# Kernel tuning notes

Hardware: AMD Instinct MI355X
Metric: run time of the kernel (lower is better)

## Reference

```python
import jax, jax.numpy as jnp
import numpy as np

B, T, D, H = 4, 1024, 1024, 16
NUM_BUCKETS = 320
MAX_DIST = 800
LN_EPS = 1e-5


def _rel_bucket(T):
    # bidirectional T5-style relative position buckets
    ctx = jnp.arange(T)[:, None]
    mem = jnp.arange(T)[None, :]
    rel = mem - ctx  # (T, T)
    half = NUM_BUCKETS // 2  # 160
    bucket = (rel > 0).astype(jnp.int32) * half
    n = jnp.abs(rel)
    max_exact = half // 2  # 80
    is_small = n < max_exact
    n_f = jnp.maximum(n, 1).astype(jnp.float32)
    large = max_exact + (
        jnp.log(n_f / max_exact) / np.log(MAX_DIST / max_exact) * (half - max_exact)
    ).astype(jnp.int32)
    large = jnp.minimum(large, half - 1)
    return bucket + jnp.where(is_small, n, large)


def setup_inputs() -> dict:
    key = jax.random.key(0)
    ks = jax.random.split(key, 12)
    s = 0.02
    return {
        "x": jax.random.normal(ks[0], (B, T, D), jnp.float32),
        "ln_w": jnp.ones((D,), jnp.float32),
        "ln_b": jnp.zeros((D,), jnp.float32),
        "wq": jax.random.normal(ks[1], (D, D), jnp.float32) * s,
        "bq": jnp.zeros((D,), jnp.float32),
        "wk": jax.random.normal(ks[2], (D, D), jnp.float32) * s,
        "bk": jnp.zeros((D,), jnp.float32),
        "wv": jax.random.normal(ks[3], (D, D), jnp.float32) * s,
        "bv": jnp.zeros((D,), jnp.float32),
        "wo": jax.random.normal(ks[4], (D, D), jnp.float32) * s,
        "bo": jnp.zeros((D,), jnp.float32),
        "rel_emb": jax.random.normal(ks[5], (NUM_BUCKETS, H), jnp.float32) * s,
        "grep_w": jax.random.normal(ks[6], (8, D // H), jnp.float32) * s,
        "grep_b": jnp.zeros((8,), jnp.float32),
        "grep_a": jnp.ones((1, H, 1, 1), jnp.float32),
    }


def reference(x, ln_w, ln_b, wq, bq, wk, bk, wv, bv, wo, bo, rel_emb, grep_w, grep_b, grep_a):
    Bb, Tt, Dd = x.shape
    hd = Dd // H
    scaling = hd ** -0.5
    # pre-norm LayerNorm
    mu = jnp.mean(x, -1, keepdims=True)
    var = jnp.mean((x - mu) ** 2, -1, keepdims=True)
    h = (x - mu) / jnp.sqrt(var + LN_EPS) * ln_w + ln_b
    # projections (q pre-scaled as in fairseq/WavLM)
    q = (h @ wq.T + bq) * scaling
    k = h @ wk.T + bk
    v = h @ wv.T + bv
    q = q.reshape(Bb, Tt, H, hd).transpose(0, 2, 1, 3)  # (B,H,T,hd)
    k = k.reshape(Bb, Tt, H, hd).transpose(0, 2, 1, 3)
    v = v.reshape(Bb, Tt, H, hd).transpose(0, 2, 1, 3)
    # bucketed relative position bias: (H, T, T)
    buckets = _rel_bucket(Tt)
    pos_bias = rel_emb[buckets].transpose(2, 0, 1)
    # gru_rel_pos gating (per batch, head, query position)
    alpha = 32.0
    ql = q * (alpha / scaling)  # undo scaling, multiply by alpha
    g = jax.nn.sigmoid((ql @ grep_w.T + grep_b).reshape(Bb, H, Tt, 2, 4).sum(-1))
    gate_a, gate_b = g[..., 0:1], g[..., 1:2]  # (B,H,T,1)
    gate = gate_a * (gate_b * grep_a - 1.0) + 2.0
    # attention
    scores = jnp.einsum('bhtd,bhsd->bhts', q, k) + gate * pos_bias[None]
    attn = jax.nn.softmax(scores, axis=-1)
    out = jnp.einsum('bhts,bhsd->bhtd', attn, v).transpose(0, 2, 1, 3).reshape(Bb, Tt, Dd)
    # output projection, dropout (identity in eval), residual
    out = out @ wo.T + bo + x
    pos_bias_out = jnp.broadcast_to(pos_bias[None], (Bb, H, Tt, Tt)).reshape(Bb * H, Tt, Tt)
    return out, pos_bias_out
```

## Files before the change

### kernel.cpp

```cpp
#include <hip/hip_runtime.h>

typedef unsigned short u16;
typedef __attribute__((ext_vector_type(8))) short short8;
typedef __attribute__((ext_vector_type(4))) float floatx4;

#define MFMA16(a, b, c) __builtin_amdgcn_mfma_f32_16x16x32_bf16(a, b, c, 0, 0, 0)

#define GLL16(gp, lp)                                                              \
  __builtin_amdgcn_global_load_lds(                                                \
      (const __attribute__((address_space(1))) void*)(gp),                         \
      (__attribute__((address_space(3))) void*)(lp), 16, 0, 0)

__device__ __forceinline__ float bf2f(u16 u) {
  return __uint_as_float(((unsigned int)u) << 16);
}
__device__ __forceinline__ u16 f2bf(float f) {
  unsigned int u = __float_as_uint(f);
  unsigned int r = (u + 0x7fffu + ((u >> 16) & 1u)) >> 16;
  return (u16)r;
}

__global__ __launch_bounds__(256) void ln_kernel(
    const float* __restrict__ x, const float* __restrict__ w, const float* __restrict__ bb,
    u16* __restrict__ hb)
{
  int wid = threadIdx.x >> 6, lane = threadIdx.x & 63;
  int row = blockIdx.x * 4 + wid;
  const float* xr = x + row * 1024 + lane * 16;
  float xs[16];
#pragma unroll
  for (int i = 0; i < 4; i++) {
    float4 v = *(const float4*)(xr + i * 4);
    xs[i * 4 + 0] = v.x; xs[i * 4 + 1] = v.y; xs[i * 4 + 2] = v.z; xs[i * 4 + 3] = v.w;
  }
  float s = 0.f, ss = 0.f;
#pragma unroll
  for (int i = 0; i < 16; i++) { s += xs[i]; ss += xs[i] * xs[i]; }
#pragma unroll
  for (int m = 1; m < 64; m <<= 1) { s += __shfl_xor(s, m, 64); ss += __shfl_xor(ss, m, 64); }
  float mu = s * (1.0f / 1024.0f);
  float var = ss * (1.0f / 1024.0f) - mu * mu;
  float rstd = rsqrtf(var + 1e-5f);
  const float* wr = w + lane * 16;
  const float* br = bb + lane * 16;
  short8 o0, o1;
#pragma unroll
  for (int i = 0; i < 8; i++) {
    o0[i] = (short)f2bf((xs[i] - mu) * rstd * wr[i] + br[i]);
    o1[i] = (short)f2bf((xs[8 + i] - mu) * rstd * wr[8 + i] + br[8 + i]);
  }
  u16* hr = hb + row * 1024 + lane * 16;
  *(short8*)hr = o0;
  *(short8*)(hr + 8) = o1;
}

__device__ __forceinline__ int rel_bucket(int t, int s) {
  int rel = s - t;
  int bucket = (rel > 0) ? 160 : 0;
  int n = (rel < 0) ? -rel : rel;
  if (n < 80) return bucket + n;
  float a = logf((float)n / 80.0f);
  float c = a / (float)2.302585092994046;
  float v = c * 80.0f;
  int large = 80 + (int)v;
  if (large > 159) large = 159;
  return bucket + large;
}

__global__ __launch_bounds__(256) void convw_kernel(
    const float* __restrict__ wq, const float* __restrict__ wk,
    const float* __restrict__ wv, const float* __restrict__ wo,
    u16* __restrict__ wb, const float* __restrict__ rel_emb, float* __restrict__ tbl)
{
  int bid = blockIdx.x;
  if (bid >= 2048) {
    int idx = (bid - 2048) * 256 + threadIdx.x;
    int h = idx & 15, ri = idx >> 4;
    float v = 0.f;
    if (ri < 2047) {
      int rel = ri - 1023;
      v = rel_emb[rel_bucket(0, rel) * 16 + h];
    }
    tbl[h * 2048 + ri] = v;
    return;
  }
  int idx = (bid * 256 + threadIdx.x) * 8;
  int seg = idx >> 20, off = idx & 1048575;
  const float* s = (seg == 0) ? wq : (seg == 1) ? wk : (seg == 2) ? wv : wo;
  float4 f0 = *(const float4*)(s + off);
  float4 f1 = *(const float4*)(s + off + 4);
  short8 o;
  o[0] = (short)f2bf(f0.x); o[1] = (short)f2bf(f0.y);
  o[2] = (short)f2bf(f0.z); o[3] = (short)f2bf(f0.w);
  o[4] = (short)f2bf(f1.x); o[5] = (short)f2bf(f1.y);
  o[6] = (short)f2bf(f1.z); o[7] = (short)f2bf(f1.w);
  *(short8*)&wb[idx] = o;
}

__global__ __launch_bounds__(256) void qkv_kernel(
    const u16* __restrict__ hb, const u16* __restrict__ wb,
    const float* __restrict__ bq, const float* __restrict__ bk, const float* __restrict__ bv,
    u16* __restrict__ qs, u16* __restrict__ kko, u16* __restrict__ vn)
{
  __shared__ __align__(16) u16 As[128 * 32];
  __shared__ __align__(16) u16 Bs[128 * 32];
  int tid = threadIdx.x;
  int wid = tid >> 6, lane = tid & 63;
  int wm = wid >> 1, wn = wid & 1;
  int l15 = lane & 15, quad = lane >> 4;
  int m0 = blockIdx.y * 128;
  int n0g = blockIdx.x * 128;
  int sec = n0g >> 10;
  int n0 = n0g & 1023;
  const u16* W = wb + sec * 1048576;
  const float* bias = (sec == 0) ? bq : ((sec == 1) ? bk : bv);

  floatx4 zero4 = {0.f, 0.f, 0.f, 0.f};
  floatx4 acc[4][4];
#pragma unroll
  for (int i = 0; i < 4; i++)
#pragma unroll
    for (int j = 0; j < 4; j++) acc[i][j] = zero4;

  int lr = tid >> 2;
  int lc = (tid & 3) * 8;
  const u16* ga0 = &hb[(m0 + lr) * 1024 + lc];
  const u16* ga1 = &hb[(m0 + lr + 64) * 1024 + lc];
  const u16* gb0 = &W[(n0 + lr) * 1024 + lc];
  const u16* gb1 = &W[(n0 + lr + 64) * 1024 + lc];
  u16* la0 = &As[lr * 32 + lc];
  u16* la1 = &As[(lr + 64) * 32 + lc];
  u16* lb0 = &Bs[lr * 32 + lc];
  u16* lb1 = &Bs[(lr + 64) * 32 + lc];

  for (int kt = 0; kt < 1024; kt += 32) {
    GLL16(ga0 + kt, la0);
    GLL16(ga1 + kt, la1);
    GLL16(gb0 + kt, lb0);
    GLL16(gb1 + kt, lb1);
    __syncthreads();
    short8 af[4], bf[4];
#pragma unroll
    for (int mi = 0; mi < 4; mi++)
      af[mi] = *(const short8*)&As[(wm * 64 + mi * 16 + l15) * 32 + quad * 8];
#pragma unroll
    for (int ni = 0; ni < 4; ni++)
      bf[ni] = *(const short8*)&Bs[(wn * 64 + ni * 16 + l15) * 32 + quad * 8];
#pragma unroll
    for (int mi = 0; mi < 4; mi++)
#pragma unroll
      for (int ni = 0; ni < 4; ni++)
        acc[mi][ni] = MFMA16(af[mi], bf[ni], acc[mi][ni]);
    __syncthreads();
  }

  int bidx = m0 >> 10;
#pragma unroll
  for (int mi = 0; mi < 4; mi++) {
#pragma unroll
    for (int ni = 0; ni < 4; ni++) {
#pragma unroll
      for (int r = 0; r < 4; r++) {
        int row = m0 + wm * 64 + mi * 16 + quad * 4 + r;
        int t = row & 1023;
        int c = n0 + wn * 64 + ni * 16 + l15;
        float val = acc[mi][ni][r] + bias[c];
        int hh = c >> 6, hp = c & 63;
        if (sec == 0) {
          val *= 0.125f;
          qs[((bidx * 16 + hh) * 1024 + t) * 64 + hp] = f2bf(val);
        } else if (sec == 1) {
          kko[((bidx * 16 + hh) * 1024 + t) * 64 + hp] = f2bf(val);
        } else {
          vn[((bidx * 16 + hh) * 1024 + t) * 64 + hp] = f2bf(val);
        }
      }
    }
  }
}

__global__ __launch_bounds__(256) void vtrans_kernel(
    const u16* __restrict__ vn, u16* __restrict__ vt)
{
  __shared__ u16 Ts[64 * 72];
  int bh = blockIdx.x >> 4;
  int t0 = (blockIdx.x & 15) * 64;
  int tid = threadIdx.x;
  int row = tid >> 2;
  int c16 = (tid & 3) * 16;
  const u16* src = vn + bh * 65536 + (t0 + row) * 64 + c16;
  *(short8*)&Ts[row * 72 + c16]     = *(const short8*)&src[0];
  *(short8*)&Ts[row * 72 + c16 + 8] = *(const short8*)&src[8];
  __syncthreads();
  short8 o0, o1;
#pragma unroll
  for (int j = 0; j < 8; j++) {
    o0[j] = (short)Ts[(c16 + j) * 72 + row];
    o1[j] = (short)Ts[(c16 + 8 + j) * 72 + row];
  }
  u16* dst = vt + bh * 65536 + row * 1024 + t0 + c16;
  *(short8*)&dst[0] = o0;
  *(short8*)&dst[8] = o1;
}

__global__ __launch_bounds__(256) void attn_kernel(
    const u16* __restrict__ qs, const u16* __restrict__ kko, const u16* __restrict__ vt,
    const float* __restrict__ gw, const float* __restrict__ gb, const float* __restrict__ ga,
    const float* __restrict__ tbl, u16* __restrict__ ao)
{
  __shared__ __align__(16) u16 Pb[4][2 * 768];
  int wid = threadIdx.x >> 6, lane = threadIdx.x & 63;
  int l15 = lane & 15, quad = lane >> 4;
  int bh = blockIdx.x;
  int b = bh >> 4, h = bh & 15;
  int q0 = blockIdx.y * 64 + wid * 16;
  const u16* Q = qs + bh * 65536;
  const u16* K = kko + bh * 65536;
  const u16* V = vt + bh * 65536;
  u16* pbase = &Pb[wid][0];

  const u16* qrow = Q + (q0 + l15) * 64;
  float e[8];
#pragma unroll
  for (int i = 0; i < 8; i++) e[i] = 0.f;
  {
    short8 qa = *(const short8*)&qrow[quad * 16];
    short8 qc = *(const short8*)&qrow[quad * 16 + 8];
#pragma unroll
    for (int jj = 0; jj < 8; jj++) {
      float qla = bf2f((u16)qa[jj]) * 256.0f;
      float qlb = bf2f((u16)qc[jj]) * 256.0f;
      int j = quad * 16 + jj;
#pragma unroll
      for (int i = 0; i < 8; i++) {
        e[i] += qla * gw[i * 64 + j];
        e[i] += qlb * gw[i * 64 + j + 8];
      }
    }
  }
#pragma unroll
  for (int i = 0; i < 8; i++) {
    e[i] += __shfl_xor(e[i], 16, 64);
    e[i] += __shfl_xor(e[i], 32, 64);
  }
  float u0 = e[0] + e[1] + e[2] + e[3] + gb[0] + gb[1] + gb[2] + gb[3];
  float u1 = e[4] + e[5] + e[6] + e[7] + gb[4] + gb[5] + gb[6] + gb[7];
  float sa = 1.0f / (1.0f + __expf(-u0));
  float sc_ = 1.0f / (1.0f + __expf(-u1));
  float gv = sa * (sc_ * ga[h] - 1.0f) + 2.0f;

  short8 qf0 = *(const short8*)&Q[(q0 + l15) * 64 + quad * 8];
  short8 qf1 = *(const short8*)&Q[(q0 + l15) * 64 + quad * 8 + 32];

  const float* tb = tbl + h * 2048 + 1023 + quad * 4 - (q0 + l15);

  float mrun = -1e30f, lrun = 0.f;
  floatx4 zero4 = {0.f, 0.f, 0.f, 0.f};
  floatx4 accO[4];
#pragma unroll
  for (int ni = 0; ni < 4; ni++) accO[ni] = zero4;

  const u16* Kr = K + l15 * 64 + quad * 8;
  short8 ka0 = *(const short8*)&Kr[0];
  short8 ka1 = *(const short8*)&Kr[32];
  short8 kb0 = *(const short8*)&Kr[16 * 64];
  short8 kb1 = *(const short8*)&Kr[16 * 64 + 32];
  float bt[8];
#pragma unroll
  for (int r = 0; r < 4; r++) { bt[r] = tb[r]; bt[4 + r] = tb[16 + r]; }

  for (int it = 0; it < 32; it++) {
    int s0 = it * 32;
    floatx4 sc0 = zero4, sc1 = zero4;
    sc0 = MFMA16(ka0, qf0, sc0);
    sc0 = MFMA16(ka1, qf1, sc0);
    sc1 = MFMA16(kb0, qf0, sc1);
    sc1 = MFMA16(kb1, qf1, sc1);

    int sn = (s0 + 32) & 1023;
    const u16* Kn = K + (sn + l15) * 64 + quad * 8;
    short8 na0 = *(const short8*)&Kn[0];
    short8 na1 = *(const short8*)&Kn[32];
    short8 nb0 = *(const short8*)&Kn[16 * 64];
    short8 nb1 = *(const short8*)&Kn[16 * 64 + 32];
    float btn[8];
#pragma unroll
    for (int r = 0; r < 4; r++) { btn[r] = tb[sn + r]; btn[4 + r] = tb[sn + 16 + r]; }
    short8 vf0 = *(const short8*)&V[(0 * 16 + l15) * 1024 + s0 + quad * 8];
    short8 vf1 = *(const short8*)&V[(1 * 16 + l15) * 1024 + s0 + quad * 8];
    short8 vf2 = *(const short8*)&V[(2 * 16 + l15) * 1024 + s0 + quad * 8];
    short8 vf3 = *(const short8*)&V[(3 * 16 + l15) * 1024 + s0 + quad * 8];

    float vv[8];
#pragma unroll
    for (int r = 0; r < 4; r++) {
      vv[r]     = sc0[r] + gv * bt[r];
      vv[4 + r] = sc1[r] + gv * bt[4 + r];
    }
    float mt = fmaxf(fmaxf(fmaxf(vv[0], vv[1]), fmaxf(vv[2], vv[3])),
                     fmaxf(fmaxf(vv[4], vv[5]), fmaxf(vv[6], vv[7])));
    mt = fmaxf(mt, __shfl_xor(mt, 16, 64));
    mt = fmaxf(mt, __shfl_xor(mt, 32, 64));
    float mnew = fmaxf(mrun, mt);
    float al = __expf(fmaxf(mrun - mnew, -80.0f));
    float p[8], ps = 0.f;
#pragma unroll
    for (int j = 0; j < 8; j++) { p[j] = __expf(vv[j] - mnew); ps += p[j]; }
    ps += __shfl_xor(ps, 16, 64);
    ps += __shfl_xor(ps, 32, 64);
    lrun = lrun * al + ps;
    mrun = mnew;

    float ar[4];
#pragma unroll
    for (int r = 0; r < 4; r++) ar[r] = __shfl(al, quad * 4 + r, 64);
#pragma unroll
    for (int ni = 0; ni < 4; ni++) {
      floatx4 t = accO[ni];
      t[0] *= ar[0]; t[1] *= ar[1]; t[2] *= ar[2]; t[3] *= ar[3];
      accO[ni] = t;
    }

    unsigned w0, w1, w2, w3;
    asm("v_cvt_pk_bf16_f32 %0, %1, %2" : "=v"(w0) : "v"(p[0]), "v"(p[1]));
    asm("v_cvt_pk_bf16_f32 %0, %1, %2" : "=v"(w1) : "v"(p[2]), "v"(p[3]));
    asm("v_cvt_pk_bf16_f32 %0, %1, %2" : "=v"(w2) : "v"(p[4]), "v"(p[5]));
    asm("v_cvt_pk_bf16_f32 %0, %1, %2" : "=v"(w3) : "v"(p[6]), "v"(p[7]));
    u16* pw = pbase + (it & 1) * 768;
    uint2 wa; wa.x = w0; wa.y = w1;
    uint2 wbv; wbv.x = w2; wbv.y = w3;
    *(uint2*)&pw[l15 * 48 + quad * 4] = wa;
    *(uint2*)&pw[l15 * 48 + 16 + quad * 4] = wbv;
    asm volatile("s_waitcnt lgkmcnt(0)" ::: "memory");
    __builtin_amdgcn_sched_barrier(0);
    short8 pf = *(const short8*)&pw[l15 * 48 + quad * 8];

    accO[0] = MFMA16(pf, vf0, accO[0]);
    accO[1] = MFMA16(pf, vf1, accO[1]);
    accO[2] = MFMA16(pf, vf2, accO[2]);
    accO[3] = MFMA16(pf, vf3, accO[3]);

    ka0 = na0; ka1 = na1; kb0 = nb0; kb1 = nb1;
#pragma unroll
    for (int j = 0; j < 8; j++) bt[j] = btn[j];
  }

#pragma unroll
  for (int r = 0; r < 4; r++) {
    float lr = __shfl(lrun, quad * 4 + r, 64);
    float rl = 1.0f / lr;
    int t = q0 + quad * 4 + r;
#pragma unroll
    for (int ni = 0; ni < 4; ni++) {
      ao[(b * 1024 + t) * 1024 + h * 64 + ni * 16 + l15] = f2bf(accO[ni][r] * rl);
    }
  }
}

__global__ __launch_bounds__(256) void oproj_kernel(
    const u16* __restrict__ ao, const u16* __restrict__ wob, const float* __restrict__ bo,
    const float* __restrict__ x, float* __restrict__ out)
{
  __shared__ __align__(16) u16 As[128 * 32];
  __shared__ __align__(16) u16 Bs[128 * 32];
  int tid = threadIdx.x;
  int wid = tid >> 6, lane = tid & 63;
  int wm = wid >> 1, wn = wid & 1;
  int l15 = lane & 15, quad = lane >> 4;
  int m0 = blockIdx.y * 128;
  int n0 = blockIdx.x * 128;

  floatx4 zero4 = {0.f, 0.f, 0.f, 0.f};
  floatx4 acc[4][4];
#pragma unroll
  for (int i = 0; i < 4; i++)
#pragma unroll
    for (int j = 0; j < 4; j++) acc[i][j] = zero4;

  int lr = tid >> 2;
  int lc = (tid & 3) * 8;
  const u16* ga0 = &ao[(m0 + lr) * 1024 + lc];
  const u16* ga1 = &ao[(m0 + lr + 64) * 1024 + lc];
  const u16* gb0 = &wob[(n0 + lr) * 1024 + lc];
  const u16* gb1 = &wob[(n0 + lr + 64) * 1024 + lc];
  u16* la0 = &As[lr * 32 + lc];
  u16* la1 = &As[(lr + 64) * 32 + lc];
  u16* lb0 = &Bs[lr * 32 + lc];
  u16* lb1 = &Bs[(lr + 64) * 32 + lc];

  for (int kt = 0; kt < 1024; kt += 32) {
    GLL16(ga0 + kt, la0);
    GLL16(ga1 + kt, la1);
    GLL16(gb0 + kt, lb0);
    GLL16(gb1 + kt, lb1);
    __syncthreads();
    short8 af[4], bf[4];
#pragma unroll
    for (int mi = 0; mi < 4; mi++)
      af[mi] = *(const short8*)&As[(wm * 64 + mi * 16 + l15) * 32 + quad * 8];
#pragma unroll
    for (int ni = 0; ni < 4; ni++)
      bf[ni] = *(const short8*)&Bs[(wn * 64 + ni * 16 + l15) * 32 + quad * 8];
#pragma unroll
    for (int mi = 0; mi < 4; mi++)
#pragma unroll
      for (int ni = 0; ni < 4; ni++)
        acc[mi][ni] = MFMA16(af[mi], bf[ni], acc[mi][ni]);
    __syncthreads();
  }

#pragma unroll
  for (int mi = 0; mi < 4; mi++) {
#pragma unroll
    for (int ni = 0; ni < 4; ni++) {
#pragma unroll
      for (int r = 0; r < 4; r++) {
        int row = m0 + wm * 64 + mi * 16 + quad * 4 + r;
        int c = n0 + wn * 64 + ni * 16 + l15;
        out[row * 1024 + c] = acc[mi][ni][r] + bo[c] + x[row * 1024 + c];
      }
    }
  }
}

__global__ __launch_bounds__(256) void bias_all_kernel(
    const float* __restrict__ rel_emb, float* __restrict__ out1)
{
  int tid = blockIdx.x * 256 + threadIdx.x;
  int t = tid >> 7;
  int s0 = (tid & 127) * 8;
  int bkt[8];
#pragma unroll
  for (int j = 0; j < 8; j++) bkt[j] = rel_bucket(t, s0 + j) * 16;
  int base_ts = t * 1024 + s0;
#pragma unroll
  for (int hh = 0; hh < 16; hh++) {
    float4 v0, v1;
    v0.x = rel_emb[bkt[0] + hh]; v0.y = rel_emb[bkt[1] + hh];
    v0.z = rel_emb[bkt[2] + hh]; v0.w = rel_emb[bkt[3] + hh];
    v1.x = rel_emb[bkt[4] + hh]; v1.y = rel_emb[bkt[5] + hh];
    v1.z = rel_emb[bkt[6] + hh]; v1.w = rel_emb[bkt[7] + hh];
    float* p = out1 + hh * 1048576 + base_ts;
    *(float4*)p = v0;              *(float4*)(p + 4) = v1;
    *(float4*)(p + 16777216) = v0; *(float4*)(p + 16777216 + 4) = v1;
    *(float4*)(p + 33554432) = v0; *(float4*)(p + 33554432 + 4) = v1;
    *(float4*)(p + 50331648) = v0; *(float4*)(p + 50331648 + 4) = v1;
  }
}

extern "C" void kernel_launch(void* const* d_in, const int* in_sizes, int n_in,
                              void* d_out, int out_size, void* d_ws, size_t ws_size,
                              hipStream_t stream) {
  const float* x    = (const float*)d_in[0];
  const float* ln_w = (const float*)d_in[1];
  const float* ln_b = (const float*)d_in[2];
  const float* wq   = (const float*)d_in[3];
  const float* bq   = (const float*)d_in[4];
  const float* wk   = (const float*)d_in[5];
  const float* bk   = (const float*)d_in[6];
  const float* wv   = (const float*)d_in[7];
  const float* bv   = (const float*)d_in[8];
  const float* wo   = (const float*)d_in[9];
  const float* bo   = (const float*)d_in[10];
  const float* rel  = (const float*)d_in[11];
  const float* gw   = (const float*)d_in[12];
  const float* gb   = (const float*)d_in[13];
  const float* ga   = (const float*)d_in[14];

  float* out0  = (float*)d_out;
  float* out1f = out0 + 4194304;

  u16* hbb  = (u16*)(out1f + 16777216);
  u16* wbb  = (u16*)(out1f + 18874368);
  u16* qsb  = (u16*)(out1f + 20971520);
  u16* kkb  = (u16*)(out1f + 23068672);
  u16* vnb  = (u16*)(out1f + 25165824);
  u16* vtb  = (u16*)(out1f + 27262976);
  u16* aob  = (u16*)(out1f + 29360128);
  float* tbl =        out1f + 31457280;

  ln_kernel<<<1024, 256, 0, stream>>>(x, ln_w, ln_b, hbb);
  convw_kernel<<<2176, 256, 0, stream>>>(wq, wk, wv, wo, wbb, rel, tbl);
  qkv_kernel<<<dim3(24, 32), 256, 0, stream>>>(hbb, wbb, bq, bk, bv, qsb, kkb, vnb);
  vtrans_kernel<<<1024, 256, 0, stream>>>(vnb, vtb);
  attn_kernel<<<dim3(64, 16), 256, 0, stream>>>(qsb, kkb, vtb, gw, gb, ga, tbl, aob);
  oproj_kernel<<<dim3(8, 32), 256, 0, stream>>>(aob, wbb + 3145728, bo, x, out0);
  bias_all_kernel<<<512, 256, 0, stream>>>(rel, out1f);
}
```

Baseline: 524.6 us.

## Merge LayerNorm into prep kernel, skip softmax rescale, use workspace scratch

Folds the LayerNorm kernel into the weight-conversion/table kernel as extra blocks, removing one launch. Adds a lazy-rescale path in attention: when the new tile max exceeds the running max by at most 8 across the wave, the accumulator rescale and max update are skipped. Intermediate buffers move to the provided workspace when it is large enough, instead of living past the end of the output buffer. The lazy rescale lets unnormalised exponentials grow by up to e^8, which trades a little precision headroom for fewer multiplies and shuffles.

```diff
diff --git a/kernel.cpp b/kernel.cpp
--- a/kernel.cpp
+++ b/kernel.cpp
@@ -18,40 +18,6 @@
   unsigned int u = __float_as_uint(f);
   unsigned int r = (u + 0x7fffu + ((u >> 16) & 1u)) >> 16;
   return (u16)r;
-}
-
-__global__ __launch_bounds__(256) void ln_kernel(
-    const float* __restrict__ x, const float* __restrict__ w, const float* __restrict__ bb,
-    u16* __restrict__ hb)
-{
-  int wid = threadIdx.x >> 6, lane = threadIdx.x & 63;
-  int row = blockIdx.x * 4 + wid;
-  const float* xr = x + row * 1024 + lane * 16;
-  float xs[16];
-#pragma unroll
-  for (int i = 0; i < 4; i++) {
-    float4 v = *(const float4*)(xr + i * 4);
-    xs[i * 4 + 0] = v.x; xs[i * 4 + 1] = v.y; xs[i * 4 + 2] = v.z; xs[i * 4 + 3] = v.w;
-  }
-  float s = 0.f, ss = 0.f;
-#pragma unroll
-  for (int i = 0; i < 16; i++) { s += xs[i]; ss += xs[i] * xs[i]; }
-#pragma unroll
-  for (int m = 1; m < 64; m <<= 1) { s += __shfl_xor(s, m, 64); ss += __shfl_xor(ss, m, 64); }
-  float mu = s * (1.0f / 1024.0f);
-  float var = ss * (1.0f / 1024.0f) - mu * mu;
-  float rstd = rsqrtf(var + 1e-5f);
-  const float* wr = w + lane * 16;
-  const float* br = bb + lane * 16;
-  short8 o0, o1;
-#pragma unroll
-  for (int i = 0; i < 8; i++) {
-    o0[i] = (short)f2bf((xs[i] - mu) * rstd * wr[i] + br[i]);
-    o1[i] = (short)f2bf((xs[8 + i] - mu) * rstd * wr[8 + i] + br[8 + i]);
-  }
-  u16* hr = hb + row * 1024 + lane * 16;
-  *(short8*)hr = o0;
-  *(short8*)(hr + 8) = o1;
 }
 
 __device__ __forceinline__ int rel_bucket(int t, int s) {
@@ -67,12 +33,45 @@
   return bucket + large;
 }
 
-__global__ __launch_bounds__(256) void convw_kernel(
+__global__ __launch_bounds__(256) void prep_kernel(
     const float* __restrict__ wq, const float* __restrict__ wk,
     const float* __restrict__ wv, const float* __restrict__ wo,
-    u16* __restrict__ wb, const float* __restrict__ rel_emb, float* __restrict__ tbl)
+    u16* __restrict__ wb, const float* __restrict__ rel_emb, float* __restrict__ tbl,
+    const float* __restrict__ x, const float* __restrict__ ln_w, const float* __restrict__ ln_b,
+    u16* __restrict__ hb)
 {
   int bid = blockIdx.x;
+  if (bid >= 2176) {
+    int wid = threadIdx.x >> 6, lane = threadIdx.x & 63;
+    int row = (bid - 2176) * 4 + wid;
+    const float* xr = x + row * 1024 + lane * 16;
+    float xs[16];
+#pragma unroll
+    for (int i = 0; i < 4; i++) {
+      float4 v = *(const float4*)(xr + i * 4);
+      xs[i * 4 + 0] = v.x; xs[i * 4 + 1] = v.y; xs[i * 4 + 2] = v.z; xs[i * 4 + 3] = v.w;
+    }
+    float s = 0.f, ss = 0.f;
+#pragma unroll
+    for (int i = 0; i < 16; i++) { s += xs[i]; ss += xs[i] * xs[i]; }
+#pragma unroll
+    for (int m = 1; m < 64; m <<= 1) { s += __shfl_xor(s, m, 64); ss += __shfl_xor(ss, m, 64); }
+    float mu = s * (1.0f / 1024.0f);
+    float var = ss * (1.0f / 1024.0f) - mu * mu;
+    float rstd = rsqrtf(var + 1e-5f);
+    const float* wr = ln_w + lane * 16;
+    const float* br = ln_b + lane * 16;
+    short8 o0, o1;
+#pragma unroll
+    for (int i = 0; i < 8; i++) {
+      o0[i] = (short)f2bf((xs[i] - mu) * rstd * wr[i] + br[i]);
+      o1[i] = (short)f2bf((xs[8 + i] - mu) * rstd * wr[8 + i] + br[8 + i]);
+    }
+    u16* hr = hb + row * 1024 + lane * 16;
+    *(short8*)hr = o0;
+    *(short8*)(hr + 8) = o1;
+    return;
+  }
   if (bid >= 2048) {
     int idx = (bid - 2048) * 256 + threadIdx.x;
     int h = idx & 15, ri = idx >> 4;
@@ -301,24 +300,32 @@
                      fmaxf(fmaxf(vv[4], vv[5]), fmaxf(vv[6], vv[7])));
     mt = fmaxf(mt, __shfl_xor(mt, 16, 64));
     mt = fmaxf(mt, __shfl_xor(mt, 32, 64));
-    float mnew = fmaxf(mrun, mt);
-    float al = __expf(fmaxf(mrun - mnew, -80.0f));
+
     float p[8], ps = 0.f;
-#pragma unroll
-    for (int j = 0; j < 8; j++) { p[j] = __expf(vv[j] - mnew); ps += p[j]; }
-    ps += __shfl_xor(ps, 16, 64);
-    ps += __shfl_xor(ps, 32, 64);
-    lrun = lrun * al + ps;
-    mrun = mnew;
-
-    float ar[4];
-#pragma unroll
-    for (int r = 0; r < 4; r++) ar[r] = __shfl(al, quad * 4 + r, 64);
-#pragma unroll
-    for (int ni = 0; ni < 4; ni++) {
-      floatx4 t = accO[ni];
-      t[0] *= ar[0]; t[1] *= ar[1]; t[2] *= ar[2]; t[3] *= ar[3];
-      accO[ni] = t;
+    if (__all(mt - mrun <= 8.0f)) {
+#pragma unroll
+      for (int j = 0; j < 8; j++) { p[j] = __expf(vv[j] - mrun); ps += p[j]; }
+      ps += __shfl_xor(ps, 16, 64);
+      ps += __shfl_xor(ps, 32, 64);
+      lrun += ps;
+    } else {
+      float mnew = fmaxf(mrun, mt);
+      float al = __expf(fmaxf(mrun - mnew, -80.0f));
+#pragma unroll
+      for (int j = 0; j < 8; j++) { p[j] = __expf(vv[j] - mnew); ps += p[j]; }
+      ps += __shfl_xor(ps, 16, 64);
+      ps += __shfl_xor(ps, 32, 64);
+      lrun = lrun * al + ps;
+      mrun = mnew;
+      float ar[4];
+#pragma unroll
+      for (int r = 0; r < 4; r++) ar[r] = __shfl(al, quad * 4 + r, 64);
+#pragma unroll
+      for (int ni = 0; ni < 4; ni++) {
+        floatx4 t = accO[ni];
+        t[0] *= ar[0]; t[1] *= ar[1]; t[2] *= ar[2]; t[3] *= ar[3];
+        accO[ni] = t;
+      }
     }
 
     unsigned w0, w1, w2, w3;
@@ -470,17 +477,19 @@
   float* out0  = (float*)d_out;
   float* out1f = out0 + 4194304;
 
-  u16* hbb  = (u16*)(out1f + 16777216);
-  u16* wbb  = (u16*)(out1f + 18874368);
-  u16* qsb  = (u16*)(out1f + 20971520);
-  u16* kkb  = (u16*)(out1f + 23068672);
-  u16* vnb  = (u16*)(out1f + 25165824);
-  u16* vtb  = (u16*)(out1f + 27262976);
-  u16* aob  = (u16*)(out1f + 29360128);
-  float* tbl =        out1f + 31457280;
-
-  ln_kernel<<<1024, 256, 0, stream>>>(x, ln_w, ln_b, hbb);
-  convw_kernel<<<2176, 256, 0, stream>>>(wq, wk, wv, wo, wbb, rel, tbl);
+  bool use_ws = (ws_size >= (size_t)(64u << 20));
+  float* scr = use_ws ? (float*)d_ws : (out1f + 16777216);
+
+  u16* hbb  = (u16*)(scr);
+  u16* wbb  = (u16*)(scr + 2097152);
+  u16* qsb  = (u16*)(scr + 4194304);
+  u16* kkb  = (u16*)(scr + 6291456);
+  u16* vnb  = (u16*)(scr + 8388608);
+  u16* vtb  = (u16*)(scr + 10485760);
+  u16* aob  = (u16*)(scr + 12582912);
+  float* tbl =        scr + 14680064;
+
+  prep_kernel<<<3200, 256, 0, stream>>>(wq, wk, wv, wo, wbb, rel, tbl, x, ln_w, ln_b, hbb);
   qkv_kernel<<<dim3(24, 32), 256, 0, stream>>>(hbb, wbb, bq, bk, bv, qsb, kkb, vnb);
   vtrans_kernel<<<1024, 256, 0, stream>>>(vnb, vtb);
   attn_kernel<<<dim3(64, 16), 256, 0, stream>>>(qsb, kkb, vtb, gw, gb, ga, tbl, aob);
```

Measured after the change: 530.3 us. About the same (+1.1%).
